# Kernel optimization log

Hardware: AMD Instinct MI355X
Metric: run time of the kernel (lower is better)

Reference implementation:

```python
import jax, jax.numpy as jnp
import numpy as np
import math

D_MODEL = 1024
N_HEADS = 16
SLOT_DIM = 64
N_SLOTS = 1024
TOP_K = 2
LN_EPS = 1e-5


def setup_inputs() -> dict:
    key = jax.random.key(0)
    ks = jax.random.split(key, 8)
    x = jax.random.normal(ks[0], (4, 2048, D_MODEL), dtype=jnp.float32)
    ln_gamma = jnp.ones((D_MODEL,), jnp.float32)
    ln_beta = jnp.zeros((D_MODEL,), jnp.float32)
    q_w = jax.random.normal(ks[1], (N_HEADS * SLOT_DIM, D_MODEL), jnp.float32) / math.sqrt(D_MODEL)
    q_b = jnp.zeros((N_HEADS * SLOT_DIM,), jnp.float32)
    slot_signatures = jax.random.normal(ks[2], (N_HEADS, N_SLOTS, SLOT_DIM), jnp.float32) * 0.5
    slot_values = jax.random.normal(ks[3], (N_HEADS, N_SLOTS, SLOT_DIM), jnp.float32) * 0.02
    out_w = jax.random.normal(ks[4], (D_MODEL, N_HEADS * SLOT_DIM), jnp.float32) / math.sqrt(N_HEADS * SLOT_DIM)
    out_b = jnp.zeros((D_MODEL,), jnp.float32)
    temperature = jnp.ones((1,), jnp.float32)
    return {"x": x, "ln_gamma": ln_gamma, "ln_beta": ln_beta, "q_w": q_w, "q_b": q_b,
            "slot_signatures": slot_signatures, "slot_values": slot_values,
            "out_w": out_w, "out_b": out_b, "temperature": temperature}


def _ternary_ste(sig):
    # forward = {-1,0,+1} quantization; backward = identity (straight-through)
    q = jnp.where(sig > 0.3, 1.0, jnp.where(sig < -0.3, -1.0, 0.0))
    return sig + jax.lax.stop_gradient(q - sig)


def reference(x, ln_gamma, ln_beta, q_w, q_b, slot_signatures, slot_values, out_w, out_b, temperature):
    B, T, D = x.shape
    # LayerNorm
    mean = jnp.mean(x, axis=-1, keepdims=True)
    var = jnp.var(x, axis=-1, keepdims=True)
    x_norm = (x - mean) * jax.lax.rsqrt(var + LN_EPS) * ln_gamma + ln_beta
    # Query projection -> [B, T, H, slot_dim]
    q = (x_norm @ q_w.T + q_b).reshape(B, T, N_HEADS, SLOT_DIM)
    sigs = _ternary_ste(slot_signatures)  # [H, S, d]
    scores = jnp.einsum('bthd,hsd->bths', q, sigs)
    scores = scores / (temperature * math.sqrt(SLOT_DIM))  # [B, T, H, S]
    # top-k routing
    topk_scores, slot_idx = jax.lax.top_k(scores, TOP_K)  # [B, T, H, K]
    weights = jax.nn.softmax(topk_scores, axis=-1)
    # gather selected slot values: [B, T, H, K, d]
    h_idx = jnp.arange(N_HEADS)[None, None, :, None]
    selected = slot_values[h_idx, slot_idx]
    read = jnp.sum(selected * weights[..., None], axis=3)  # [B, T, H, d]
    read = read.reshape(B, T, N_HEADS * SLOT_DIM)
    out = read @ out_w.T + out_b
    return x + out
```

## Files before the change

### kernel.cpp

```cpp
#include <hip/hip_runtime.h>

typedef unsigned short u16;
typedef unsigned int   u32;
typedef float f32x4  __attribute__((ext_vector_type(4)));
typedef float f32x16 __attribute__((ext_vector_type(16)));
typedef __bf16 bf16x8 __attribute__((ext_vector_type(8)));

__device__ __forceinline__ u16 f2bf(float f){
  u32 u = __float_as_uint(f);
  u += 0x7fffu + ((u >> 16) & 1u);
  return (u16)(u >> 16);
}

__device__ __forceinline__ void gld16(const void* g, void* l){
  __builtin_amdgcn_global_load_lds((const __attribute__((address_space(1))) u32*)g,
                                   (__attribute__((address_space(3))) u32*)l, 16, 0, 0);
}

__global__ __launch_bounds__(256) void convert_kernel(
    const float* __restrict__ qw, const float* __restrict__ ow,
    const float* __restrict__ sg,
    u16* __restrict__ qwb, u16* __restrict__ owb, u16* __restrict__ sgb){
  int i = (blockIdx.x * 256 + threadIdx.x) * 4;
  f32x4 a = *(const f32x4*)(qw + i);
  f32x4 b = *(const f32x4*)(ow + i);
  f32x4 s = *(const f32x4*)(sg + i);
  uint2 pa, pb, ps;
  pa.x = (u32)f2bf(a[0]) | ((u32)f2bf(a[1]) << 16);
  pa.y = (u32)f2bf(a[2]) | ((u32)f2bf(a[3]) << 16);
  pb.x = (u32)f2bf(b[0]) | ((u32)f2bf(b[1]) << 16);
  pb.y = (u32)f2bf(b[2]) | ((u32)f2bf(b[3]) << 16);
  float t0 = (s[0] > 0.3f) ? 1.0f : ((s[0] < -0.3f) ? -1.0f : 0.0f);
  float t1 = (s[1] > 0.3f) ? 1.0f : ((s[1] < -0.3f) ? -1.0f : 0.0f);
  float t2 = (s[2] > 0.3f) ? 1.0f : ((s[2] < -0.3f) ? -1.0f : 0.0f);
  float t3 = (s[3] > 0.3f) ? 1.0f : ((s[3] < -0.3f) ? -1.0f : 0.0f);
  ps.x = (u32)f2bf(t0) | ((u32)f2bf(t1) << 16);
  ps.y = (u32)f2bf(t2) | ((u32)f2bf(t3) << 16);
  *(uint2*)(qwb + i) = pa;
  *(uint2*)(owb + i) = pb;
  *(uint2*)(sgb + i) = ps;
}

__global__ __launch_bounds__(256) void ln_kernel(
    const float* __restrict__ x, const float* __restrict__ g,
    const float* __restrict__ b, u16* __restrict__ xn){
  const int tid = threadIdx.x, lane = tid & 63, w = tid >> 6;
  const int t = blockIdx.x * 4 + w;
  const float* xr = x + (size_t)t * 1024;
  f32x4 v[4];
  #pragma unroll
  for (int j = 0; j < 4; ++j) v[j] = *(const f32x4*)(xr + j * 256 + lane * 4);
  float s = 0.f, ss = 0.f;
  #pragma unroll
  for (int j = 0; j < 4; ++j)
    #pragma unroll
    for (int e = 0; e < 4; ++e){ s += v[j][e]; ss += v[j][e] * v[j][e]; }
  #pragma unroll
  for (int off = 32; off; off >>= 1){
    s  += __shfl_xor(s, off);
    ss += __shfl_xor(ss, off);
  }
  float mean = s * (1.0f / 1024.0f);
  float var  = ss * (1.0f / 1024.0f) - mean * mean;
  float rs   = rsqrtf(var + 1e-5f);
  #pragma unroll
  for (int j = 0; j < 4; ++j){
    f32x4 gv = *(const f32x4*)(g + j * 256 + lane * 4);
    f32x4 bv = *(const f32x4*)(b + j * 256 + lane * 4);
    float y0 = (v[j][0]-mean)*rs*gv[0]+bv[0];
    float y1 = (v[j][1]-mean)*rs*gv[1]+bv[1];
    float y2 = (v[j][2]-mean)*rs*gv[2]+bv[2];
    float y3 = (v[j][3]-mean)*rs*gv[3]+bv[3];
    uint2 pk;
    pk.x = (u32)f2bf(y0) | ((u32)f2bf(y1) << 16);
    pk.y = (u32)f2bf(y2) | ((u32)f2bf(y3) << 16);
    *(uint2*)(xn + (size_t)t * 1024 + j * 256 + lane * 4) = pk;
  }
}

__global__ __launch_bounds__(256, 2) void gemm_bt(
    const u16* __restrict__ A, const u16* __restrict__ B,
    const float* __restrict__ bias, const float* __restrict__ resid,
    float* __restrict__ outf, u16* __restrict__ outb, int mode){
  __shared__ u16 As[2][128 * 64];
  __shared__ u16 Bs[2][128 * 64];
  const int tid = threadIdx.x;
  const int b = blockIdx.x;
  const int m0 = ((b & 7) * 8 + ((b >> 3) & 7)) * 128;
  const int n0 = (b >> 6) * 128;
  const int w = tid >> 6, lane = tid & 63, lm = lane & 15, quad = lane >> 4;
  const int wm = (w & 1) * 64, wn = (w >> 1) * 64;
  const int lr = lane >> 3;
  const int lg = (lane & 7) ^ lr;
  const f32x4 fz = {0.f, 0.f, 0.f, 0.f};
  f32x4 acc[4][4];
  #pragma unroll
  for (int i = 0; i < 4; ++i)
    #pragma unroll
    for (int j = 0; j < 4; ++j) acc[i][j] = fz;

  const u16* gA = A + (size_t)(m0 + w * 32 + lr) * 1024 + lg * 8;
  const u16* gB = B + (size_t)(n0 + w * 32 + lr) * 1024 + lg * 8;
  const int lbase = (w * 32) * 64;
  const int sw = lm & 7;

  auto stage = [&](int kt, int bb){
    #pragma unroll
    for (int sub = 0; sub < 4; ++sub){
      gld16(gA + (size_t)(sub * 8) * 1024 + kt * 64, &As[bb][lbase + sub * 8 * 64]);
      gld16(gB + (size_t)(sub * 8) * 1024 + kt * 64, &Bs[bb][lbase + sub * 8 * 64]);
    }
  };

  stage(0, 0);
  for (int kt = 0; kt < 16; ++kt){
    __syncthreads();
    if (kt < 15) stage(kt + 1, (kt + 1) & 1);
    const u16* as = As[kt & 1];
    const u16* bs = Bs[kt & 1];
    #pragma unroll
    for (int kk = 0; kk < 2; ++kk){
      const int ch = ((quad + kk * 4) ^ sw) * 8;
      bf16x8 afr[4], bfr[4];
      #pragma unroll
      for (int i = 0; i < 4; ++i)
        afr[i] = *(const bf16x8*)(&as[(wm + i * 16 + lm) * 64 + ch]);
      #pragma unroll
      for (int j = 0; j < 4; ++j)
        bfr[j] = *(const bf16x8*)(&bs[(wn + j * 16 + lm) * 64 + ch]);
      #pragma unroll
      for (int i = 0; i < 4; ++i)
        #pragma unroll
        for (int j = 0; j < 4; ++j)
          acc[i][j] = __builtin_amdgcn_mfma_f32_16x16x32_bf16(afr[i], bfr[j], acc[i][j], 0, 0, 0);
    }
  }

  #pragma unroll
  for (int i = 0; i < 4; ++i){
    #pragma unroll
    for (int r = 0; r < 4; ++r){
      int grow = m0 + wm + i * 16 + quad * 4 + r;
      #pragma unroll
      for (int j = 0; j < 4; ++j){
        int gcol = n0 + wn + j * 16 + lm;
        float v = acc[i][j][r] + bias[gcol];
        if (mode){
          v += resid[(size_t)grow * 1024 + gcol];
          outf[(size_t)grow * 1024 + gcol] = v;
        } else {
          outb[(size_t)grow * 1024 + gcol] = f2bf(v);
        }
      }
    }
  }
}

#define MERGE2(V1,I1,V2,I2, o1,oi1,o2,oi2) {                      \
    u32   cb2 = (o2 > V2) ? oi2 : I2;                             \
    float c2  = fmaxf(V2, o2);                                    \
    u32   nb1 = (o1 > V1) ? oi1 : I1;                             \
    float n1  = fmaxf(V1, o1);                                    \
    float n2  = __builtin_amdgcn_fmed3f(V1, o1, c2);              \
    u32   nb2 = (n2 == o1) ? oi1 : ((n2 == V1) ? I1 : cb2);       \
    V1 = n1; I1 = nb1; V2 = n2; I2 = nb2; }

__global__ __launch_bounds__(512) void route2_kernel(
    const u16* __restrict__ q, const u16* __restrict__ sig,
    const float* __restrict__ V, const float* __restrict__ temp,
    u16* __restrict__ rd){
  const int b = blockIdx.x;
  const int h = b & 15, chunk = b >> 4;
  const int t0 = chunk * 256;
  const int tid = threadIdx.x, w = tid >> 6, lane = tid & 63;
  const int col = lane & 31, half = lane >> 5;

  __shared__ uint4 sv[2][8][32];

  const float tsc = 1.0f / (temp[0] * 8.0f);

  const u16* sigh = sig + (size_t)h * 65536;
  bf16x8 sfr[4][4];
  #pragma unroll
  for (int blk = 0; blk < 4; ++blk){
    const u16* sp = sigh + (size_t)(w * 128 + blk * 32 + col) * 64 + half * 8;
    #pragma unroll
    for (int c = 0; c < 4; ++c)
      sfr[blk][c] = *(const bf16x8*)(sp + c * 16);
  }

  u32 rk[16];
  #pragma unroll
  for (int r = 0; r < 16; ++r) rk[r] = (u32)((r & 3) + 8 * (r >> 2) + 4 * half);

  const u16* qbase = q + (size_t)h * 64 + half * 8;
  bf16x8 qf[4], qn[4];
  {
    const u16* qp = qbase + (size_t)(t0 + col) * 1024;
    #pragma unroll
    for (int c = 0; c < 4; ++c) qf[c] = *(const bf16x8*)(qp + c * 16);
  }

  const f32x16 fzero = {};
  for (int tt = 0; tt < 8; ++tt){
    {
      int tn = (tt < 7) ? tt + 1 : 7;
      const u16* qp = qbase + (size_t)(t0 + tn * 32 + col) * 1024;
      #pragma unroll
      for (int c = 0; c < 4; ++c) qn[c] = *(const bf16x8*)(qp + c * 16);
    }
    float v1 = -3.0e38f, v2 = -3.0e38f; u32 i1 = 0, i2 = 0;
    #pragma unroll
    for (int blk = 0; blk < 4; ++blk){
      f32x16 acc;
      acc = __builtin_amdgcn_mfma_f32_32x32x16_bf16(sfr[blk][0], qf[0], fzero, 0, 0, 0);
      acc = __builtin_amdgcn_mfma_f32_32x32x16_bf16(sfr[blk][1], qf[1], acc, 0, 0, 0);
      acc = __builtin_amdgcn_mfma_f32_32x32x16_bf16(sfr[blk][2], qf[2], acc, 0, 0, 0);
      acc = __builtin_amdgcn_mfma_f32_32x32x16_bf16(sfr[blk][3], qf[3], acc, 0, 0, 0);
      float k[16];
      #pragma unroll
      for (int r = 0; r < 16; ++r)
        k[r] = __uint_as_float((__float_as_uint(acc[r]) & 0xFFFFFFE0u) | rk[r]);
      float a1[5], a2[5];
      #pragma unroll
      for (int i = 0; i < 5; ++i){
        float x = k[3*i], y = k[3*i+1], z = k[3*i+2];
        a1[i] = fmaxf(fmaxf(x, y), z);
        a2[i] = __builtin_amdgcn_fmed3f(x, y, z);
      }
      float m1 = fmaxf(a1[0], a1[1]);
      float m2 = __builtin_amdgcn_fmed3f(a1[0], a1[1], fmaxf(a2[0], a2[1]));
      float n1 = fmaxf(a1[2], a1[3]);
      float n2 = __builtin_amdgcn_fmed3f(a1[2], a1[3], fmaxf(a2[2], a2[3]));
      float o1 = fmaxf(a1[4], k[15]);
      float o2 = __builtin_amdgcn_fmed3f(a1[4], k[15], a2[4]);
      float p1 = fmaxf(m1, n1);
      float p2 = __builtin_amdgcn_fmed3f(m1, n1, fmaxf(m2, n2));
      float f1 = fmaxf(p1, o1);
      float f2 = __builtin_amdgcn_fmed3f(p1, o1, fmaxf(p2, o2));
      u32 bt = (u32)blk;
      MERGE2(v1, i1, v2, i2, f1, bt, f2, bt);
    }
    #pragma unroll
    for (int c = 0; c < 4; ++c) qf[c] = qn[c];
    {
      float x1 = __shfl_xor(v1, 32);
      float x2 = __shfl_xor(v2, 32);
      u32 xi1 = (u32)__shfl_xor((int)i1, 32);
      u32 xi2 = (u32)__shfl_xor((int)i2, 32);
      MERGE2(v1, i1, v2, i2, x1, xi1, x2, xi2);
    }
    if (half == 0){
      uint4 pkt;
      pkt.x = __float_as_uint(v1);
      pkt.y = __float_as_uint(v2);
      pkt.z = (u32)(w * 128) + i1 * 32 + (__float_as_uint(v1) & 31u);
      pkt.w = (u32)(w * 128) + i2 * 32 + (__float_as_uint(v2) & 31u);
      sv[tt & 1][w][col] = pkt;
    }
    __syncthreads();
    int tk = w * 4 + (lane >> 4);
    uint4 pa = sv[tt & 1][0][tk];
    float V1 = __uint_as_float(pa.x), V2 = __uint_as_float(pa.y);
    u32 I1 = pa.z, I2 = pa.w;
    #pragma unroll
    for (int ws = 1; ws < 8; ++ws){
      uint4 pb = sv[tt & 1][ws][tk];
      float q1 = __uint_as_float(pb.x), q2 = __uint_as_float(pb.y);
      u32 j1 = pb.z, j2 = pb.w;
      MERGE2(V1, I1, V2, I2, q1, j1, q2, j2);
    }
    float sc1 = __uint_as_float(__float_as_uint(V1) & 0xFFFFFFE0u);
    float sc2 = __uint_as_float(__float_as_uint(V2) & 0xFFFFFFE0u);
    float ex = __expf((sc2 - sc1) * tsc);
    float iw = 1.0f / (1.0f + ex);
    float W1 = iw, W2 = ex * iw;
    int token = t0 + tt * 32 + tk, d0 = (lane & 15) * 4;
    f32x4 xa = *(const f32x4*)(V + ((size_t)h * 1024 + I1) * 64 + d0);
    f32x4 xb = *(const f32x4*)(V + ((size_t)h * 1024 + I2) * 64 + d0);
    uint2 o;
    o.x = (u32)f2bf(W1*xa[0]+W2*xb[0]) | ((u32)f2bf(W1*xa[1]+W2*xb[1]) << 16);
    o.y = (u32)f2bf(W1*xa[2]+W2*xb[2]) | ((u32)f2bf(W1*xa[3]+W2*xb[3]) << 16);
    *(uint2*)(rd + (size_t)token * 1024 + h * 64 + d0) = o;
  }
}

extern "C" void kernel_launch(void* const* d_in, const int* in_sizes, int n_in,
                              void* d_out, int out_size, void* d_ws, size_t ws_size,
                              hipStream_t stream){
  const float* x    = (const float*)d_in[0];
  const float* lng  = (const float*)d_in[1];
  const float* lnb  = (const float*)d_in[2];
  const float* qw   = (const float*)d_in[3];
  const float* qb   = (const float*)d_in[4];
  const float* sig  = (const float*)d_in[5];
  const float* sv   = (const float*)d_in[6];
  const float* ow   = (const float*)d_in[7];
  const float* ob   = (const float*)d_in[8];
  const float* temp = (const float*)d_in[9];
  float* out = (float*)d_out;

  char* ws = (char*)d_ws;
  u16* xn   = (u16*)(ws);
  u16* qwb  = (u16*)(ws + 16777216);
  u16* owb  = (u16*)(ws + 16777216 + 2097152);
  u16* sgb  = (u16*)(ws + 16777216 + 2 * 2097152);
  u16* qb16 = (u16*)(ws + 16777216 + 3 * 2097152);
  u16* rdb  = xn;

  convert_kernel<<<1024, 256, 0, stream>>>(qw, ow, sig, qwb, owb, sgb);
  ln_kernel<<<2048, 256, 0, stream>>>(x, lng, lnb, xn);
  gemm_bt<<<512, 256, 0, stream>>>(xn, qwb, qb, nullptr, nullptr, qb16, 0);
  route2_kernel<<<512, 512, 0, stream>>>(qb16, sgb, sv, temp, rdb);
  gemm_bt<<<512, 256, 0, stream>>>(rdb, owb, ob, x, out, nullptr, 1);
}
```

Before: 212.1 us.

## Restructure routing kernel: per-wave slot streaming with 16x16 MFMA and shuffle top-2

Replaces the routing kernel so that each wave owns 64 tokens and streams all 1024 slot signatures through registers using 16x16x32 MFMAs. It keeps a running top-2 per token with a packed 10-bit slot index in the score's low mantissa bits, and the cross-block LDS merge and __syncthreads are replaced by a lane-shuffle reduction. This removes shared memory and block synchronisation and reduces signature register footprint. The cost is more global/L2 signature traffic per wave and coarser score precision, since ten mantissa bits are now truncated instead of five, which could alter ties in top-k selection.

```diff
diff --git a/kernel.cpp b/kernel.cpp
--- a/kernel.cpp
+++ b/kernel.cpp
@@ -3,7 +3,6 @@
 typedef unsigned short u16;
 typedef unsigned int   u32;
 typedef float f32x4  __attribute__((ext_vector_type(4)));
-typedef float f32x16 __attribute__((ext_vector_type(16)));
 typedef __bf16 bf16x8 __attribute__((ext_vector_type(8)));
 
 __device__ __forceinline__ u16 f2bf(float f){
@@ -156,132 +155,111 @@
   }
 }
 
-#define MERGE2(V1,I1,V2,I2, o1,oi1,o2,oi2) {                      \
-    u32   cb2 = (o2 > V2) ? oi2 : I2;                             \
-    float c2  = fmaxf(V2, o2);                                    \
-    u32   nb1 = (o1 > V1) ? oi1 : I1;                             \
-    float n1  = fmaxf(V1, o1);                                    \
-    float n2  = __builtin_amdgcn_fmed3f(V1, o1, c2);              \
-    u32   nb2 = (n2 == o1) ? oi1 : ((n2 == V1) ? I1 : cb2);       \
-    V1 = n1; I1 = nb1; V2 = n2; I2 = nb2; }
-
-__global__ __launch_bounds__(512) void route2_kernel(
+__global__ __launch_bounds__(256) void route3_kernel(
     const u16* __restrict__ q, const u16* __restrict__ sig,
     const float* __restrict__ V, const float* __restrict__ temp,
     u16* __restrict__ rd){
-  const int b = blockIdx.x;
-  const int h = b & 15, chunk = b >> 4;
-  const int t0 = chunk * 256;
+  const int h = blockIdx.y;
   const int tid = threadIdx.x, w = tid >> 6, lane = tid & 63;
-  const int col = lane & 31, half = lane >> 5;
-
-  __shared__ uint4 sv[2][8][32];
-
-  const float tsc = 1.0f / (temp[0] * 8.0f);
-
-  const u16* sigh = sig + (size_t)h * 65536;
-  bf16x8 sfr[4][4];
-  #pragma unroll
-  for (int blk = 0; blk < 4; ++blk){
-    const u16* sp = sigh + (size_t)(w * 128 + blk * 32 + col) * 64 + half * 8;
-    #pragma unroll
-    for (int c = 0; c < 4; ++c)
-      sfr[blk][c] = *(const bf16x8*)(sp + c * 16);
-  }
-
-  u32 rk[16];
-  #pragma unroll
-  for (int r = 0; r < 16; ++r) rk[r] = (u32)((r & 3) + 8 * (r >> 2) + 4 * half);
-
-  const u16* qbase = q + (size_t)h * 64 + half * 8;
-  bf16x8 qf[4], qn[4];
-  {
-    const u16* qp = qbase + (size_t)(t0 + col) * 1024;
-    #pragma unroll
-    for (int c = 0; c < 4; ++c) qf[c] = *(const bf16x8*)(qp + c * 16);
-  }
-
-  const f32x16 fzero = {};
-  for (int tt = 0; tt < 8; ++tt){
-    {
-      int tn = (tt < 7) ? tt + 1 : 7;
-      const u16* qp = qbase + (size_t)(t0 + tn * 32 + col) * 1024;
-      #pragma unroll
-      for (int c = 0; c < 4; ++c) qn[c] = *(const bf16x8*)(qp + c * 16);
-    }
-    float v1 = -3.0e38f, v2 = -3.0e38f; u32 i1 = 0, i2 = 0;
-    #pragma unroll
-    for (int blk = 0; blk < 4; ++blk){
-      f32x16 acc;
-      acc = __builtin_amdgcn_mfma_f32_32x32x16_bf16(sfr[blk][0], qf[0], fzero, 0, 0, 0);
-      acc = __builtin_amdgcn_mfma_f32_32x32x16_bf16(sfr[blk][1], qf[1], acc, 0, 0, 0);
-      acc = __builtin_amdgcn_mfma_f32_32x32x16_bf16(sfr[blk][2], qf[2], acc, 0, 0, 0);
-      acc = __builtin_amdgcn_mfma_f32_32x32x16_bf16(sfr[blk][3], qf[3], acc, 0, 0, 0);
-      float k[16];
-      #pragma unroll
-      for (int r = 0; r < 16; ++r)
-        k[r] = __uint_as_float((__float_as_uint(acc[r]) & 0xFFFFFFE0u) | rk[r]);
-      float a1[5], a2[5];
-      #pragma unroll
-      for (int i = 0; i < 5; ++i){
-        float x = k[3*i], y = k[3*i+1], z = k[3*i+2];
-        a1[i] = fmaxf(fmaxf(x, y), z);
-        a2[i] = __builtin_amdgcn_fmed3f(x, y, z);
-      }
-      float m1 = fmaxf(a1[0], a1[1]);
-      float m2 = __builtin_amdgcn_fmed3f(a1[0], a1[1], fmaxf(a2[0], a2[1]));
-      float n1 = fmaxf(a1[2], a1[3]);
-      float n2 = __builtin_amdgcn_fmed3f(a1[2], a1[3], fmaxf(a2[2], a2[3]));
-      float o1 = fmaxf(a1[4], k[15]);
-      float o2 = __builtin_amdgcn_fmed3f(a1[4], k[15], a2[4]);
-      float p1 = fmaxf(m1, n1);
-      float p2 = __builtin_amdgcn_fmed3f(m1, n1, fmaxf(m2, n2));
-      float f1 = fmaxf(p1, o1);
-      float f2 = __builtin_amdgcn_fmed3f(p1, o1, fmaxf(p2, o2));
-      u32 bt = (u32)blk;
-      MERGE2(v1, i1, v2, i2, f1, bt, f2, bt);
-    }
-    #pragma unroll
-    for (int c = 0; c < 4; ++c) qf[c] = qn[c];
-    {
-      float x1 = __shfl_xor(v1, 32);
-      float x2 = __shfl_xor(v2, 32);
-      u32 xi1 = (u32)__shfl_xor((int)i1, 32);
-      u32 xi2 = (u32)__shfl_xor((int)i2, 32);
-      MERGE2(v1, i1, v2, i2, x1, xi1, x2, xi2);
-    }
-    if (half == 0){
-      uint4 pkt;
-      pkt.x = __float_as_uint(v1);
-      pkt.y = __float_as_uint(v2);
-      pkt.z = (u32)(w * 128) + i1 * 32 + (__float_as_uint(v1) & 31u);
-      pkt.w = (u32)(w * 128) + i2 * 32 + (__float_as_uint(v2) & 31u);
-      sv[tt & 1][w][col] = pkt;
-    }
-    __syncthreads();
-    int tk = w * 4 + (lane >> 4);
-    uint4 pa = sv[tt & 1][0][tk];
-    float V1 = __uint_as_float(pa.x), V2 = __uint_as_float(pa.y);
-    u32 I1 = pa.z, I2 = pa.w;
-    #pragma unroll
-    for (int ws = 1; ws < 8; ++ws){
-      uint4 pb = sv[tt & 1][ws][tk];
-      float q1 = __uint_as_float(pb.x), q2 = __uint_as_float(pb.y);
-      u32 j1 = pb.z, j2 = pb.w;
-      MERGE2(V1, I1, V2, I2, q1, j1, q2, j2);
-    }
-    float sc1 = __uint_as_float(__float_as_uint(V1) & 0xFFFFFFE0u);
-    float sc2 = __uint_as_float(__float_as_uint(V2) & 0xFFFFFFE0u);
-    float ex = __expf((sc2 - sc1) * tsc);
-    float iw = 1.0f / (1.0f + ex);
-    float W1 = iw, W2 = ex * iw;
-    int token = t0 + tt * 32 + tk, d0 = (lane & 15) * 4;
-    f32x4 xa = *(const f32x4*)(V + ((size_t)h * 1024 + I1) * 64 + d0);
-    f32x4 xb = *(const f32x4*)(V + ((size_t)h * 1024 + I2) * 64 + d0);
-    uint2 o;
-    o.x = (u32)f2bf(W1*xa[0]+W2*xb[0]) | ((u32)f2bf(W1*xa[1]+W2*xb[1]) << 16);
-    o.y = (u32)f2bf(W1*xa[2]+W2*xb[2]) | ((u32)f2bf(W1*xa[3]+W2*xb[3]) << 16);
-    *(uint2*)(rd + (size_t)token * 1024 + h * 64 + d0) = o;
+  const int lm = lane & 15, quad = lane >> 4;
+  const int t0 = blockIdx.x * 256 + w * 64;
+
+  bf16x8 qf[4][2];
+  #pragma unroll
+  for (int s = 0; s < 4; ++s){
+    const u16* qp = q + (size_t)(t0 + s * 16 + lm) * 1024 + h * 64 + quad * 8;
+    qf[s][0] = *(const bf16x8*)(qp);
+    qf[s][1] = *(const bf16x8*)(qp + 32);
+  }
+
+  const u16* sp = sig + (size_t)h * 65536 + lm * 64 + quad * 8;
+  bf16x8 c0 = *(const bf16x8*)(sp);
+  bf16x8 c1 = *(const bf16x8*)(sp + 32);
+  bf16x8 n0 = *(const bf16x8*)(sp + 1024);
+  bf16x8 n1 = *(const bf16x8*)(sp + 1024 + 32);
+  sp += 2048;
+
+  const f32x4 fz = {0.f, 0.f, 0.f, 0.f};
+  const u32 MASK = 0xFFFFFC00u;
+  float v1[4], v2[4];
+  #pragma unroll
+  for (int s = 0; s < 4; ++s){ v1[s] = -3.0e38f; v2[s] = -3.0e38f; }
+  u32 rk0 = (u32)(quad * 4), rk1 = rk0 + 1, rk2 = rk0 + 2, rk3 = rk0 + 3;
+
+  for (int t = 0; t < 64; ++t){
+    #pragma unroll
+    for (int s = 0; s < 4; ++s){
+      f32x4 acc = __builtin_amdgcn_mfma_f32_16x16x32_bf16(c0, qf[s][0], fz, 0, 0, 0);
+      acc       = __builtin_amdgcn_mfma_f32_16x16x32_bf16(c1, qf[s][1], acc, 0, 0, 0);
+      float k0 = __uint_as_float((__float_as_uint(acc[0]) & MASK) | rk0);
+      float k1 = __uint_as_float((__float_as_uint(acc[1]) & MASK) | rk1);
+      float k2 = __uint_as_float((__float_as_uint(acc[2]) & MASK) | rk2);
+      float k3 = __uint_as_float((__float_as_uint(acc[3]) & MASK) | rk3);
+      float o;
+      o = v1[s]; v1[s] = fmaxf(o, k0); v2[s] = __builtin_amdgcn_fmed3f(o, v2[s], k0);
+      o = v1[s]; v1[s] = fmaxf(o, k1); v2[s] = __builtin_amdgcn_fmed3f(o, v2[s], k1);
+      o = v1[s]; v1[s] = fmaxf(o, k2); v2[s] = __builtin_amdgcn_fmed3f(o, v2[s], k2);
+      o = v1[s]; v1[s] = fmaxf(o, k3); v2[s] = __builtin_amdgcn_fmed3f(o, v2[s], k3);
+    }
+    c0 = n0; c1 = n1;
+    if (t < 62){
+      n0 = *(const bf16x8*)(sp);
+      n1 = *(const bf16x8*)(sp + 32);
+      sp += 1024;
+    }
+    rk0 += 16u; rk1 += 16u; rk2 += 16u; rk3 += 16u;
+  }
+
+  #pragma unroll
+  for (int off = 16; off <= 32; off <<= 1){
+    #pragma unroll
+    for (int s = 0; s < 4; ++s){
+      float o1 = __shfl_xor(v1[s], off);
+      float o2 = __shfl_xor(v2[s], off);
+      float ov = v1[s];
+      v1[s] = fmaxf(ov, o1);
+      v2[s] = __builtin_amdgcn_fmed3f(ov, o1, fmaxf(v2[s], o2));
+    }
+  }
+
+  float a1 = (quad & 1) ? v1[1] : v1[0], b1 = (quad & 1) ? v1[3] : v1[2];
+  float a2 = (quad & 1) ? v2[1] : v2[0], b2 = (quad & 1) ? v2[3] : v2[2];
+  float V1 = (quad & 2) ? b1 : a1;
+  float V2 = (quad & 2) ? b2 : a2;
+  u32 u1 = __float_as_uint(V1), u2 = __float_as_uint(V2);
+  int I1 = (int)(u1 & 1023u), I2 = (int)(u2 & 1023u);
+  float s1 = __uint_as_float(u1 & MASK);
+  float s2 = __uint_as_float(u2 & MASK);
+  float tsc = 1.0f / (temp[0] * 8.0f);
+  float ex = __expf((s2 - s1) * tsc);
+  float iw = 1.0f / (1.0f + ex);
+  float W1 = iw, W2 = ex * iw;
+
+  const float* va = V + ((size_t)h * 1024 + I1) * 64;
+  const float* vb = V + ((size_t)h * 1024 + I2) * 64;
+  u16* dst = rd + (size_t)(t0 + lane) * 1024 + h * 64;
+  #pragma unroll
+  for (int g = 0; g < 4; ++g){
+    f32x4 xa = *(const f32x4*)(va + g * 16);
+    f32x4 xb = *(const f32x4*)(va + g * 16 + 4);
+    f32x4 xc = *(const f32x4*)(va + g * 16 + 8);
+    f32x4 xd = *(const f32x4*)(va + g * 16 + 12);
+    f32x4 ya = *(const f32x4*)(vb + g * 16);
+    f32x4 yb = *(const f32x4*)(vb + g * 16 + 4);
+    f32x4 yc = *(const f32x4*)(vb + g * 16 + 8);
+    f32x4 yd = *(const f32x4*)(vb + g * 16 + 12);
+    uint4 o;
+    o.x = (u32)f2bf(W1*xa[0]+W2*ya[0]) | ((u32)f2bf(W1*xa[1]+W2*ya[1]) << 16);
+    o.y = (u32)f2bf(W1*xa[2]+W2*ya[2]) | ((u32)f2bf(W1*xa[3]+W2*ya[3]) << 16);
+    o.z = (u32)f2bf(W1*xb[0]+W2*yb[0]) | ((u32)f2bf(W1*xb[1]+W2*yb[1]) << 16);
+    o.w = (u32)f2bf(W1*xb[2]+W2*yb[2]) | ((u32)f2bf(W1*xb[3]+W2*yb[3]) << 16);
+    uint4 p;
+    p.x = (u32)f2bf(W1*xc[0]+W2*yc[0]) | ((u32)f2bf(W1*xc[1]+W2*yc[1]) << 16);
+    p.y = (u32)f2bf(W1*xc[2]+W2*yc[2]) | ((u32)f2bf(W1*xc[3]+W2*yc[3]) << 16);
+    p.z = (u32)f2bf(W1*xd[0]+W2*yd[0]) | ((u32)f2bf(W1*xd[1]+W2*yd[1]) << 16);
+    p.w = (u32)f2bf(W1*xd[2]+W2*yd[2]) | ((u32)f2bf(W1*xd[3]+W2*yd[3]) << 16);
+    *(uint4*)(dst + g * 16) = o;
+    *(uint4*)(dst + g * 16 + 8) = p;
   }
 }
 
@@ -311,6 +289,6 @@
   convert_kernel<<<1024, 256, 0, stream>>>(qw, ow, sig, qwb, owb, sgb);
   ln_kernel<<<2048, 256, 0, stream>>>(x, lng, lnb, xn);
   gemm_bt<<<512, 256, 0, stream>>>(xn, qwb, qb, nullptr, nullptr, qb16, 0);
-  route2_kernel<<<512, 512, 0, stream>>>(qb16, sgb, sv, temp, rdb);
+  route3_kernel<<<dim3(32, 16), 256, 0, stream>>>(qb16, sgb, sv, temp, rdb);
   gemm_bt<<<512, 256, 0, stream>>>(rdb, owb, ob, x, out, nullptr, 1);
 }
```

New measurement: 216.3 us. Within noise of the previous version (+2.0%).
